# Kernel optimization log

Measured on AMD Instinct MI355X. Metric: run time of the kernel, lower is better.

## Reference

```python
import jax, jax.numpy as jnp
import numpy as np

SIGMA = 0.1

def setup_inputs() -> dict:
    key = jax.random.key(0)
    k1, k2, k3 = jax.random.split(key, 3)
    B = 16384
    risk_scores = jax.random.normal(k1, (B,), dtype=jnp.float32)
    times = jax.random.uniform(k2, (B,), dtype=jnp.float32)
    events = jax.random.randint(k3, (B,), 0, 2, dtype=jnp.int32)
    return {"risk_scores": risk_scores, "times": times, "events": events}

def reference(risk_scores, times, events):
    # mask[i, j] = (times[i] < times[j]) and (events[i] == 1)
    mask = (times[:, None] < times[None, :]) & (events[:, None] == 1)  # [B, B] bool
    maskf = mask.astype(risk_scores.dtype)
    # diff[i, j] = risk_scores[j] - risk_scores[i]
    diff = risk_scores[None, :] - risk_scores[:, None]  # [B, B]
    loss = jnp.sum(jax.nn.sigmoid(diff / SIGMA) * maskf)
    count = jnp.sum(maskf)
    return loss / (count + 1e-06)
```

## Files before the change

kernel.cpp:

```cpp
#include <hip/hip_runtime.h>


#define BLOCK 256
#define RPT 8
#define ROWS_PER_TILE (BLOCK * RPT)
#define JTILE 64
#define NCOLGRP 256
#define GRID_MAIN 1024

__device__ __forceinline__ float fast_exp2(float x) { return __builtin_amdgcn_exp2f(x); }
__device__ __forceinline__ float fast_rcp(float x)  { return __builtin_amdgcn_rcpf(x); }
__device__ __forceinline__ float clamp60(float x)   { return fminf(fmaxf(x, -60.0f), 60.0f); }

__global__ __launch_bounds__(BLOCK) void k_compact(
    const float* __restrict__ r, const float* __restrict__ t,
    const int* __restrict__ ev, int B, float kscale,
    int* __restrict__ cursor,
    float2* __restrict__ sI, float2* __restrict__ sJ) {
    const int tid = threadIdx.x;
    int g = blockIdx.x * BLOCK + tid;
    if (g >= B) return;
    float tv = t[g];
    float s  = clamp60(r[g] * kscale);
    sJ[g] = make_float2(fast_exp2(-s), tv);
    bool pred = (ev[g] == 1);
    unsigned long long bal = __ballot(pred);
    int lane = tid & 63, wid = tid >> 6;
    int before = __popcll(bal & ((1ull << lane) - 1ull));
    int wcnt = __popcll(bal);
    __shared__ int wbase[BLOCK / 64];
    if (lane == 0) wbase[wid] = wcnt;
    __syncthreads();
    if (tid == 0) {
        int c0 = wbase[0], c1 = wbase[1], c2 = wbase[2], c3 = wbase[3];
        int b0 = atomicAdd(cursor, (c0 + c1) + (c2 + c3));
        wbase[0] = b0; wbase[1] = b0 + c0; wbase[2] = b0 + c0 + c1;
        wbase[3] = b0 + c0 + c1 + c2;
    }
    __syncthreads();
    if (pred) sI[wbase[wid] + before] = make_float2(fast_exp2(s), tv);
}

__global__ __launch_bounds__(BLOCK) void k_main(
    const float2* __restrict__ sI, const float2* __restrict__ sJ,
    const int* __restrict__ nactive_g,
    float* __restrict__ pL, unsigned int* __restrict__ pC) {

    const int tid = threadIdx.x;
    const int nactive = *nactive_g;
    const int nrc = (nactive + ROWS_PER_TILE - 1) / ROWS_PER_TILE;
    const int ntiles = nrc * NCOLGRP;

    __shared__ float2 tile[JTILE];

    float lsum = 0.0f;
    int   csum = 0;

    for (int tix = blockIdx.x; tix < ntiles; tix += gridDim.x) {
        int rc = tix >> 8;
        int cg = tix & (NCOLGRP - 1);

        float E[RPT], T[RPT];
        int rbase = rc * ROWS_PER_TILE;
#pragma unroll
        for (int k = 0; k < RPT; ++k) {
            int rr = rbase + tid + (k << 8);
            if (rr < nactive) { float2 f = sI[rr]; E[k] = f.x; T[k] = f.y; }
            else              { E[k] = 1.0f; T[k] = 3.0f; }
        }

        __syncthreads();
        if (tid < JTILE) tile[tid] = sJ[(cg << 6) + tid];
        __syncthreads();

        float l[4] = {0.f, 0.f, 0.f, 0.f};
        int   c[4] = {0, 0, 0, 0};
#pragma unroll 4
        for (int jj = 0; jj < JTILE; ++jj) {
            float2 q = tile[jj];
            float F = q.x, tj = q.y;
#pragma unroll
            for (int g2 = 0; g2 < 4; ++g2) {
                float u = __builtin_fmaf(E[2*g2],   F, 1.0f);
                float v = __builtin_fmaf(E[2*g2+1], F, 1.0f);
                float p = fminf(u * v, 3.0e38f);
                float rp = fast_rcp(p);
                bool m0 = T[2*g2]   < tj;
                bool m1 = T[2*g2+1] < tj;
                float num = (m0 ? v : 0.0f) + (m1 ? u : 0.0f);
                l[g2] = __builtin_fmaf(num, rp, l[g2]);
                c[g2] += m0 + m1;
            }
        }
        lsum += (l[0] + l[1]) + (l[2] + l[3]);
        csum += (c[0] + c[1]) + (c[2] + c[3]);
    }

#pragma unroll
    for (int off = 32; off > 0; off >>= 1) {
        lsum += __shfl_down(lsum, off);
        csum += __shfl_down(csum, off);
    }
    __shared__ float lw[BLOCK / 64];
    __shared__ int   cw[BLOCK / 64];
    int wid = tid >> 6;
    if ((tid & 63) == 0) { lw[wid] = lsum; cw[wid] = csum; }
    __syncthreads();
    if (tid == 0) {
        pL[blockIdx.x] = (lw[0] + lw[1]) + (lw[2] + lw[3]);
        pC[blockIdx.x] = (unsigned)((cw[0] + cw[1]) + (cw[2] + cw[3]));
    }
}

__global__ __launch_bounds__(BLOCK) void k_finalize(
    const float* __restrict__ pL, const unsigned int* __restrict__ pC,
    int n, float* __restrict__ out) {
    double l = 0.0, c = 0.0;
    for (int i = threadIdx.x; i < n; i += BLOCK) {
        l += (double)pL[i];
        c += (double)pC[i];
    }
#pragma unroll
    for (int off = 32; off > 0; off >>= 1) {
        l += __shfl_down(l, off);
        c += __shfl_down(c, off);
    }
    __shared__ double lw[BLOCK / 64], cw[BLOCK / 64];
    int wid = threadIdx.x >> 6;
    if ((threadIdx.x & 63) == 0) { lw[wid] = l; cw[wid] = c; }
    __syncthreads();
    if (threadIdx.x == 0) {
        double L = (lw[0] + lw[1]) + (lw[2] + lw[3]);
        double C = (cw[0] + cw[1]) + (cw[2] + cw[3]);
        out[0] = (float)(L / (C + 1e-6));
    }
}

extern "C" void kernel_launch(void* const* d_in, const int* in_sizes, int n_in,
                              void* d_out, int out_size, void* d_ws, size_t ws_size,
                              hipStream_t stream) {
    const float* r  = (const float*)d_in[0];
    const float* t  = (const float*)d_in[1];
    const int*   ev = (const int*)d_in[2];
    float* out = (float*)d_out;
    const int B = in_sizes[0];

    const float SIGMA = 0.1f;
    const float LOG2E = 1.4426950408889634f;
    const float kscale = LOG2E / SIGMA;

    char* ws = (char*)d_ws;
    int* cursor = (int*)ws;
    float2* sI  = (float2*)(ws + 4096);
    float2* sJ  = sI + B;
    float*  pL  = (float*)(sJ + B);
    unsigned int* pC = (unsigned int*)(pL + GRID_MAIN);

    const int nblk = (B + BLOCK - 1) / BLOCK;

    hipMemsetAsync(ws, 0, 64, stream);
    k_compact<<<nblk, BLOCK, 0, stream>>>(r, t, ev, B, kscale, cursor, sI, sJ);
    k_main<<<GRID_MAIN, BLOCK, 0, stream>>>(sI, sJ, cursor, pL, pC);
    k_finalize<<<1, BLOCK, 0, stream>>>(pL, pC, GRID_MAIN, out);
}
```

Baseline: 40.62 us.

## Bucket-sort by time to skip empty tiles and drop masks in full tiles

Times are bucketed with a histogram, scan and scatter so that rows and columns come out roughly sorted, and per-chunk bucket ranges are recorded. The main kernel skips tiles whose column buckets all lie below the row buckets and uses a compare-free path for tiles that are fully masked. This removes about half the pairwise work, but it adds three extra kernel launches, including a serial single-block scan. The bucket layout assumes times lie in [0,1), which holds for the test inputs; other values are clamped into edge buckets, so results stay correct but pruning becomes less effective.

```diff
diff --git a/kernel.cpp b/kernel.cpp
--- a/kernel.cpp
+++ b/kernel.cpp
@@ -1,55 +1,102 @@
 #include <hip/hip_runtime.h>
 
 
+#define NB 1024
 #define BLOCK 256
 #define RPT 8
-#define ROWS_PER_TILE (BLOCK * RPT)
+#define CHUNK (BLOCK * RPT)
+#define MAXRC 8
 #define JTILE 64
-#define NCOLGRP 256
+#define NPG 256
 #define GRID_MAIN 1024
 
 __device__ __forceinline__ float fast_exp2(float x) { return __builtin_amdgcn_exp2f(x); }
 __device__ __forceinline__ float fast_rcp(float x)  { return __builtin_amdgcn_rcpf(x); }
 __device__ __forceinline__ float clamp60(float x)   { return fminf(fmaxf(x, -60.0f), 60.0f); }
-
-__global__ __launch_bounds__(BLOCK) void k_compact(
+__device__ __forceinline__ int bucket_of(float tv) {
+    int b = (int)(tv * (float)NB);
+    return min(max(b, 0), NB - 1);
+}
+
+__global__ __launch_bounds__(BLOCK) void k_pre(
+    const float* __restrict__ t, const int* __restrict__ ev, int B,
+    int* __restrict__ histI, int* __restrict__ histJ) {
+    int g = blockIdx.x * BLOCK + threadIdx.x;
+    if (g >= B) return;
+    int b = bucket_of(t[g]);
+    atomicAdd(&histJ[b], 1);
+    if (ev[g] == 1) atomicAdd(&histI[b], 1);
+}
+
+__global__ __launch_bounds__(1024) void k_scan(
+    const int* __restrict__ histI, const int* __restrict__ histJ,
+    int* __restrict__ curI, int* __restrict__ curJ,
+    int* __restrict__ rcLo, int* __restrict__ rcHi,
+    int* __restrict__ jpLo, int* __restrict__ jpHi,
+    int* __restrict__ nactive_g) {
+
+    const int tid = threadIdx.x;
+    __shared__ int sA[NB], sB[NB];
+    __shared__ int rcLo_s[MAXRC], rcHi_s[MAXRC];
+    __shared__ int jpLo_s[NPG], jpHi_s[NPG];
+
+    int cI = histI[tid], cJ = histJ[tid];
+    sA[tid] = cI; sB[tid] = cJ;
+    if (tid < MAXRC) { rcLo_s[tid] = 0x7fffffff; rcHi_s[tid] = -1; }
+    if (tid < NPG)   { jpLo_s[tid] = 0x7fffffff; jpHi_s[tid] = -1; }
+    __syncthreads();
+    for (int off = 1; off < NB; off <<= 1) {
+        int a = (tid >= off) ? sA[tid - off] : 0;
+        int b = (tid >= off) ? sB[tid - off] : 0;
+        __syncthreads();
+        sA[tid] += a; sB[tid] += b;
+        __syncthreads();
+    }
+    int exI = sA[tid] - cI, exJ = sB[tid] - cJ;
+    curI[tid] = exI; curJ[tid] = exJ;
+    if (tid == NB - 1) *nactive_g = sA[NB - 1];
+    if (cI > 0) {
+        int c0 = exI >> 11, c1 = (exI + cI - 1) >> 11;
+        for (int c = c0; c <= c1; ++c) { atomicMin(&rcLo_s[c], tid); atomicMax(&rcHi_s[c], tid); }
+    }
+    if (cJ > 0) {
+        int p0 = exJ >> 6, p1 = (exJ + cJ - 1) >> 6;
+        for (int p = p0; p <= p1; ++p) { atomicMin(&jpLo_s[p], tid); atomicMax(&jpHi_s[p], tid); }
+    }
+    __syncthreads();
+    if (tid < MAXRC) { rcLo[tid] = rcLo_s[tid]; rcHi[tid] = rcHi_s[tid]; }
+    if (tid < NPG)   { jpLo[tid] = jpLo_s[tid]; jpHi[tid] = jpHi_s[tid]; }
+}
+
+__global__ __launch_bounds__(BLOCK) void k_scatter(
     const float* __restrict__ r, const float* __restrict__ t,
     const int* __restrict__ ev, int B, float kscale,
-    int* __restrict__ cursor,
+    int* __restrict__ curI, int* __restrict__ curJ,
     float2* __restrict__ sI, float2* __restrict__ sJ) {
-    const int tid = threadIdx.x;
-    int g = blockIdx.x * BLOCK + tid;
+    int g = blockIdx.x * BLOCK + threadIdx.x;
     if (g >= B) return;
     float tv = t[g];
     float s  = clamp60(r[g] * kscale);
-    sJ[g] = make_float2(fast_exp2(-s), tv);
-    bool pred = (ev[g] == 1);
-    unsigned long long bal = __ballot(pred);
-    int lane = tid & 63, wid = tid >> 6;
-    int before = __popcll(bal & ((1ull << lane) - 1ull));
-    int wcnt = __popcll(bal);
-    __shared__ int wbase[BLOCK / 64];
-    if (lane == 0) wbase[wid] = wcnt;
-    __syncthreads();
-    if (tid == 0) {
-        int c0 = wbase[0], c1 = wbase[1], c2 = wbase[2], c3 = wbase[3];
-        int b0 = atomicAdd(cursor, (c0 + c1) + (c2 + c3));
-        wbase[0] = b0; wbase[1] = b0 + c0; wbase[2] = b0 + c0 + c1;
-        wbase[3] = b0 + c0 + c1 + c2;
-    }
-    __syncthreads();
-    if (pred) sI[wbase[wid] + before] = make_float2(fast_exp2(s), tv);
+    int b = bucket_of(tv);
+    int pj = atomicAdd(&curJ[b], 1);
+    sJ[pj] = make_float2(fast_exp2(-s), tv);
+    if (ev[g] == 1) {
+        int pi = atomicAdd(&curI[b], 1);
+        sI[pi] = make_float2(fast_exp2(s), tv);
+    }
 }
 
 __global__ __launch_bounds__(BLOCK) void k_main(
     const float2* __restrict__ sI, const float2* __restrict__ sJ,
+    const int* __restrict__ rcLo, const int* __restrict__ rcHi,
+    const int* __restrict__ jpLo, const int* __restrict__ jpHi,
     const int* __restrict__ nactive_g,
     float* __restrict__ pL, unsigned int* __restrict__ pC) {
 
     const int tid = threadIdx.x;
     const int nactive = *nactive_g;
-    const int nrc = (nactive + ROWS_PER_TILE - 1) / ROWS_PER_TILE;
-    const int ntiles = nrc * NCOLGRP;
+    const int nrc = (nactive + CHUNK - 1) / CHUNK;
+    const int ntiles = nrc * NPG;
 
     __shared__ float2 tile[JTILE];
 
@@ -58,42 +105,64 @@
 
     for (int tix = blockIdx.x; tix < ntiles; tix += gridDim.x) {
         int rc = tix >> 8;
-        int cg = tix & (NCOLGRP - 1);
+        int cg = tix & (NPG - 1);
+        int rl = rcLo[rc], rh = rcHi[rc];
+        int jh = jpHi[cg];
+        if (jh < rl) continue;
+        int jl = jpLo[cg];
 
         float E[RPT], T[RPT];
-        int rbase = rc * ROWS_PER_TILE;
+        int nv = 0;
+        int rbase = rc * CHUNK;
 #pragma unroll
         for (int k = 0; k < RPT; ++k) {
             int rr = rbase + tid + (k << 8);
-            if (rr < nactive) { float2 f = sI[rr]; E[k] = f.x; T[k] = f.y; }
-            else              { E[k] = 1.0f; T[k] = 3.0f; }
+            if (rr < nactive) { float2 f = sI[rr]; E[k] = f.x; T[k] = f.y; ++nv; }
+            else              { E[k] = 0.0f; T[k] = 3.0f; }
         }
 
         __syncthreads();
         if (tid < JTILE) tile[tid] = sJ[(cg << 6) + tid];
         __syncthreads();
 
-        float l[4] = {0.f, 0.f, 0.f, 0.f};
-        int   c[4] = {0, 0, 0, 0};
+        if (jl > rh) {
+            float l[4] = {0.f, 0.f, 0.f, 0.f};
 #pragma unroll 4
-        for (int jj = 0; jj < JTILE; ++jj) {
-            float2 q = tile[jj];
-            float F = q.x, tj = q.y;
-#pragma unroll
-            for (int g2 = 0; g2 < 4; ++g2) {
-                float u = __builtin_fmaf(E[2*g2],   F, 1.0f);
-                float v = __builtin_fmaf(E[2*g2+1], F, 1.0f);
-                float p = fminf(u * v, 3.0e38f);
-                float rp = fast_rcp(p);
-                bool m0 = T[2*g2]   < tj;
-                bool m1 = T[2*g2+1] < tj;
-                float num = (m0 ? v : 0.0f) + (m1 ? u : 0.0f);
-                l[g2] = __builtin_fmaf(num, rp, l[g2]);
-                c[g2] += m0 + m1;
+            for (int jj = 0; jj < JTILE; ++jj) {
+                float F = tile[jj].x;
+#pragma unroll
+                for (int g2 = 0; g2 < 4; ++g2) {
+                    float u = __builtin_fmaf(E[2*g2],   F, 1.0f);
+                    float v = __builtin_fmaf(E[2*g2+1], F, 1.0f);
+                    float rp = fast_rcp(u * v);
+                    l[g2] = __builtin_fmaf(u + v, rp, l[g2]);
+                }
             }
+            lsum += ((l[0] + l[1]) + (l[2] + l[3]))
+                  - (float)((RPT - nv) << 6);
+            csum += nv << 6;
+        } else {
+            float l[4] = {0.f, 0.f, 0.f, 0.f};
+            int   c[4] = {0, 0, 0, 0};
+#pragma unroll 4
+            for (int jj = 0; jj < JTILE; ++jj) {
+                float2 q = tile[jj];
+                float F = q.x, tj = q.y;
+#pragma unroll
+                for (int g2 = 0; g2 < 4; ++g2) {
+                    float u = __builtin_fmaf(E[2*g2],   F, 1.0f);
+                    float v = __builtin_fmaf(E[2*g2+1], F, 1.0f);
+                    float rp = fast_rcp(u * v);
+                    bool m0 = T[2*g2]   < tj;
+                    bool m1 = T[2*g2+1] < tj;
+                    float num = (m0 ? v : 0.0f) + (m1 ? u : 0.0f);
+                    l[g2] = __builtin_fmaf(num, rp, l[g2]);
+                    c[g2] += m0 + m1;
+                }
+            }
+            lsum += (l[0] + l[1]) + (l[2] + l[3]);
+            csum += (c[0] + c[1]) + (c[2] + c[3]);
         }
-        lsum += (l[0] + l[1]) + (l[2] + l[3]);
-        csum += (c[0] + c[1]) + (c[2] + c[3]);
     }
 
 #pragma unroll
@@ -150,16 +219,28 @@
     const float kscale = LOG2E / SIGMA;
 
     char* ws = (char*)d_ws;
-    int* cursor = (int*)ws;
-    float2* sI  = (float2*)(ws + 4096);
-    float2* sJ  = sI + B;
-    float*  pL  = (float*)(sJ + B);
-    unsigned int* pC = (unsigned int*)(pL + GRID_MAIN);
+    int* histI = (int*)(ws + 0);
+    int* histJ = (int*)(ws + 4096);
+    int* curI  = (int*)(ws + 8192);
+    int* curJ  = (int*)(ws + 12288);
+    int* rcLo  = (int*)(ws + 16384);
+    int* rcHi  = (int*)(ws + 16448);
+    int* jpLo  = (int*)(ws + 16512);
+    int* jpHi  = (int*)(ws + 17536);
+    int* nactive_g = (int*)(ws + 18560);
+    float2* sI = (float2*)(ws + 20480);
+    float2* sJ = (float2*)(ws + 20480 + 131072);
+    float*  pL = (float*)(ws + 20480 + 262144);
+    unsigned int* pC = (unsigned int*)((char*)pL + GRID_MAIN * 4);
 
     const int nblk = (B + BLOCK - 1) / BLOCK;
 
-    hipMemsetAsync(ws, 0, 64, stream);
-    k_compact<<<nblk, BLOCK, 0, stream>>>(r, t, ev, B, kscale, cursor, sI, sJ);
-    k_main<<<GRID_MAIN, BLOCK, 0, stream>>>(sI, sJ, cursor, pL, pC);
+    hipMemsetAsync(ws, 0, 8192, stream);
+    k_pre<<<nblk, BLOCK, 0, stream>>>(t, ev, B, histI, histJ);
+    k_scan<<<1, 1024, 0, stream>>>(histI, histJ, curI, curJ,
+                                   rcLo, rcHi, jpLo, jpHi, nactive_g);
+    k_scatter<<<nblk, BLOCK, 0, stream>>>(r, t, ev, B, kscale, curI, curJ, sI, sJ);
+    k_main<<<GRID_MAIN, BLOCK, 0, stream>>>(sI, sJ, rcLo, rcHi, jpLo, jpHi,
+                                            nactive_g, pL, pC);
     k_finalize<<<1, BLOCK, 0, stream>>>(pL, pC, GRID_MAIN, out);
 }
```

Result: slower. 47.41 us (+16.7%).
